# Kernel optimization log

Hardware: AMD Instinct MI355X
Metric: run time of the kernel (lower is better)

## Reference

```python
import jax, jax.numpy as jnp
import numpy as np

B, N, D = 16, 2048, 64

def setup_inputs() -> dict:
    key = jax.random.key(0)
    kq, kk, kv = jax.random.split(key, 3)
    queries = jax.random.normal(kq, (B, N, D), dtype=jnp.float32)
    keys = jax.random.normal(kk, (B, N, D), dtype=jnp.float32)
    values = jax.random.normal(kv, (B, N, D), dtype=jnp.float32)
    scaling_factor = jnp.asarray(np.sqrt(D), dtype=jnp.float32)
    return {"queries": queries, "keys": keys, "values": values, "scaling_factor": scaling_factor}

def reference(queries, keys, values, scaling_factor):
    # scores: [B, N, N] = Q K^T / scale
    scores = jnp.einsum('bqd,bkd->bqk', queries, keys) / scaling_factor
    atn = jax.nn.softmax(scores, axis=2)
    return jnp.einsum('bqk,bkd->bqd', atn, values)
```

## Files before the change

### kernel.cpp

```cpp
#include <hip/hip_runtime.h>
#include <hip/hip_bf16.h>

#define BATCH 16
#define SEQ 2048
#define DIM 64

typedef __attribute__((ext_vector_type(8))) __bf16 bf16x8;
typedef __attribute__((ext_vector_type(8))) unsigned short u16x8;
typedef __attribute__((ext_vector_type(4))) unsigned int u32x4;
typedef __attribute__((ext_vector_type(16))) float f32x16;

#if __has_builtin(__builtin_amdgcn_exp2f)
#define EXP2F(x) __builtin_amdgcn_exp2f(x)
#else
#define EXP2F(x) __expf(0.69314718055994531f * (x))
#endif

__device__ __forceinline__ unsigned short f2bf_hw(float f) {
    __bf16 h = (__bf16)f;
    return __builtin_bit_cast(unsigned short, h);
}

__device__ __forceinline__ unsigned int pk_bf16(float lo, float hi) {
    unsigned int a = f2bf_hw(lo), b = f2bf_hw(hi);
    return a | (b << 16);
}

__device__ __forceinline__ bf16x8 ld_bf8_g(const unsigned short* p) {
    u16x8 u = *(const u16x8*)p;
    return __builtin_bit_cast(bf16x8, u);
}

__global__ __launch_bounds__(256)
void preconvert_kv(const float* __restrict__ K, const float* __restrict__ V,
                   unsigned short* __restrict__ Ks, unsigned short* __restrict__ Vts) {
    __shared__ float vt[128 * 65];
    const int tid = threadIdx.x;
    if (blockIdx.x < 256) {
        const int b = blockIdx.x >> 4;
        const int t = blockIdx.x & 15;
        const float* src = K + ((size_t)(b * SEQ + t * 128)) * DIM;
        unsigned short* dst = Ks + ((size_t)(b * 16 + t)) * 8192;
        #pragma unroll
        for (int p = 0; p < 4; ++p) {
            const int cid = p * 256 + tid;
            const int key = cid >> 3, g = cid & 7;
            const int d0 = (g >> 1) * 16 + (g & 1) * 8;
            float4 x0 = *(const float4*)(src + key * DIM + d0);
            float4 x1 = *(const float4*)(src + key * DIM + d0 + 4);
            u16x8 o;
            o[0] = f2bf_hw(x0.x); o[1] = f2bf_hw(x0.y); o[2] = f2bf_hw(x0.z); o[3] = f2bf_hw(x0.w);
            o[4] = f2bf_hw(x1.x); o[5] = f2bf_hw(x1.y); o[6] = f2bf_hw(x1.z); o[7] = f2bf_hw(x1.w);
            *(u16x8*)(dst + (g * 128 + key) * 8) = o;
        }
    } else {
        const int vb = blockIdx.x - 256;
        const int b = vb >> 4;
        const int t = vb & 15;
        const float* src = V + ((size_t)(b * SEQ + t * 128)) * DIM;
        #pragma unroll
        for (int p = 0; p < 8; ++p) {
            const int f = p * 256 + tid;
            const int row = f >> 4, c4 = (f & 15) << 2;
            float4 x = *(const float4*)(src + row * DIM + c4);
            vt[row * 65 + c4 + 0] = x.x; vt[row * 65 + c4 + 1] = x.y;
            vt[row * 65 + c4 + 2] = x.z; vt[row * 65 + c4 + 3] = x.w;
        }
        __syncthreads();
        unsigned short* dst = Vts + ((size_t)(b * 16 + t)) * 8192;
        #pragma unroll
        for (int p = 0; p < 4; ++p) {
            const int cid = p * 256 + tid;
            const int g = cid >> 6, d = cid & 63;
            const int k0 = (g >> 1) * 16 + (g & 1) * 8;
            u16x8 o;
            #pragma unroll
            for (int j = 0; j < 8; ++j) o[j] = f2bf_hw(vt[(k0 + j) * 65 + d]);
            *(u16x8*)(dst + (g * 64 + d) * 8) = o;
        }
    }
}

__global__ __launch_bounds__(256, 2)
void attn_flash_kernel(const float* __restrict__ Q,
                       const unsigned short* __restrict__ Ks,
                       const unsigned short* __restrict__ Vts,
                       const float* __restrict__ scaling,
                       float* __restrict__ O) {
    __shared__ float comb[3 * 64 * 66];

    const int tid  = threadIdx.x;
    const int w    = tid >> 6;
    const int lane = tid & 63;
    const int m    = lane & 31;
    const int h    = lane >> 5;

    const int x  = blockIdx.x;
    const int b  = ((x & 7) << 1) | ((x >> 3) & 1);
    const int q0 = (x >> 4) * 64;

    const float csc = 1.4426950408889634f / scaling[0];

    bf16x8 aq0[4], aq1[4];
    #pragma unroll
    for (int s = 0; s < 2; ++s) {
        const float* qsrc = Q + ((size_t)(b * SEQ + q0 + s * 32 + m)) * DIM + h * 8;
        #pragma unroll
        for (int c = 0; c < 4; ++c) {
            float4 x0 = *(const float4*)(qsrc + c * 16);
            float4 x1 = *(const float4*)(qsrc + c * 16 + 4);
            u32x4 pk;
            pk[0] = pk_bf16(x0.x * csc, x0.y * csc);
            pk[1] = pk_bf16(x0.z * csc, x0.w * csc);
            pk[2] = pk_bf16(x1.x * csc, x1.y * csc);
            pk[3] = pk_bf16(x1.z * csc, x1.w * csc);
            (s ? aq1 : aq0)[c] = __builtin_bit_cast(bf16x8, pk);
        }
    }

    f32x16 Oacc0[2], Oacc1[2];
    #pragma unroll
    for (int dt = 0; dt < 2; ++dt)
        #pragma unroll
        for (int r = 0; r < 16; ++r) { Oacc0[dt][r] = 0.f; Oacc1[dt][r] = 0.f; }
    float psum0 = 0.f, psum1 = 0.f;

    const unsigned short* Kbase = Ks + ((size_t)(b * 16 + w * 4)) * 8192;
    const unsigned short* Vbase = Vts + ((size_t)(b * 16 + w * 4)) * 8192;

    bf16x8 kc[4];
    #pragma unroll
    for (int c = 0; c < 4; ++c)
        kc[c] = ld_bf8_g(&Kbase[((c * 2 + h) * 128 + m) * 8]);

    #pragma unroll 1
    for (int st = 0; st < 16; ++st) {
        const int it = st >> 2, t = st & 3;
        const unsigned short* Vt = Vbase + (size_t)it * 8192;

        f32x16 S0, S1;
        #pragma unroll
        for (int r = 0; r < 16; ++r) { S0[r] = 0.f; S1[r] = 0.f; }
        #pragma unroll
        for (int c = 0; c < 4; ++c) {
            S0 = __builtin_amdgcn_mfma_f32_32x32x16_bf16(kc[c], aq0[c], S0, 0, 0, 0);
            S1 = __builtin_amdgcn_mfma_f32_32x32x16_bf16(kc[c], aq1[c], S1, 0, 0, 0);
        }

        const int stn = (st < 15) ? st + 1 : 15;
        const unsigned short* Ktn = Kbase + (size_t)(stn >> 2) * 8192;
        const int tn = stn & 3;
        bf16x8 kn[4];
        #pragma unroll
        for (int c = 0; c < 4; ++c)
            kn[c] = ld_bf8_g(&Ktn[((c * 2 + h) * 128 + tn * 32 + m) * 8]);

        bf16x8 bv[2][2];
        #pragma unroll
        for (int c2 = 0; c2 < 2; ++c2)
            #pragma unroll
            for (int dt = 0; dt < 2; ++dt)
                bv[c2][dt] = ld_bf8_g(&Vt[(((2 * t + c2) * 2 + h) * 64 + dt * 32 + m) * 8]);

        unsigned int d0a[8], d0b[8], dsa[8], dsb[8];
        #pragma unroll
        for (int k = 0; k < 4; ++k) {
            float a0 = EXP2F(S0[4 * k + 0]), a1 = EXP2F(S0[4 * k + 1]);
            float a2 = EXP2F(S0[4 * k + 2]), a3 = EXP2F(S0[4 * k + 3]);
            psum0 += (a0 + a1) + (a2 + a3);
            d0a[2 * k + 0] = pk_bf16(a0, a1);
            d0a[2 * k + 1] = pk_bf16(a2, a3);
            float b0 = EXP2F(S1[4 * k + 0]), b1 = EXP2F(S1[4 * k + 1]);
            float b2 = EXP2F(S1[4 * k + 2]), b3 = EXP2F(S1[4 * k + 3]);
            psum1 += (b0 + b1) + (b2 + b3);
            d0b[2 * k + 0] = pk_bf16(b0, b1);
            d0b[2 * k + 1] = pk_bf16(b2, b3);
        }
        #pragma unroll
        for (int i = 0; i < 8; ++i) {
            dsa[i] = (unsigned int)__shfl_xor((int)d0a[i], 32);
            dsb[i] = (unsigned int)__shfl_xor((int)d0b[i], 32);
        }
        #pragma unroll
        for (int c2 = 0; c2 < 2; ++c2) {
            u32x4 bw0, bw1;
            bw0[0] = h ? dsa[4 * c2 + 2] : d0a[4 * c2 + 0];
            bw0[1] = h ? dsa[4 * c2 + 3] : d0a[4 * c2 + 1];
            bw0[2] = h ? d0a[4 * c2 + 2] : dsa[4 * c2 + 0];
            bw0[3] = h ? d0a[4 * c2 + 3] : dsa[4 * c2 + 1];
            bw1[0] = h ? dsb[4 * c2 + 2] : d0b[4 * c2 + 0];
            bw1[1] = h ? dsb[4 * c2 + 3] : d0b[4 * c2 + 1];
            bw1[2] = h ? d0b[4 * c2 + 2] : dsb[4 * c2 + 0];
            bw1[3] = h ? d0b[4 * c2 + 3] : dsb[4 * c2 + 1];
            bf16x8 pb0 = __builtin_bit_cast(bf16x8, bw0);
            bf16x8 pb1 = __builtin_bit_cast(bf16x8, bw1);
            #pragma unroll
            for (int dt = 0; dt < 2; ++dt) {
                Oacc0[dt] = __builtin_amdgcn_mfma_f32_32x32x16_bf16(bv[c2][dt], pb0, Oacc0[dt], 0, 0, 0);
                Oacc1[dt] = __builtin_amdgcn_mfma_f32_32x32x16_bf16(bv[c2][dt], pb1, Oacc1[dt], 0, 0, 0);
            }
        }

        #pragma unroll
        for (int c = 0; c < 4; ++c) kc[c] = kn[c];
    }

    float l0 = psum0 + __shfl_xor(psum0, 32);
    float l1 = psum1 + __shfl_xor(psum1, 32);
    if (w > 0) {
        float* dst = comb + ((w - 1) * 64 + lane) * 66;
        #pragma unroll
        for (int dt = 0; dt < 2; ++dt)
            #pragma unroll
            for (int r = 0; r < 16; ++r) {
                dst[dt * 16 + r]      = Oacc0[dt][r];
                dst[33 + dt * 16 + r] = Oacc1[dt][r];
            }
        dst[32] = l0;
        dst[65] = l1;
    }
    __syncthreads();
    if (w == 0) {
        const float* p0 = comb + (0 * 64 + lane) * 66;
        const float* p1 = comb + (1 * 64 + lane) * 66;
        const float* p2 = comb + (2 * 64 + lane) * 66;
        const float invl0 = 1.0f / (l0 + p0[32] + p1[32] + p2[32]);
        const float invl1 = 1.0f / (l1 + p0[65] + p1[65] + p2[65]);
        float* orow0 = O + ((size_t)(b * SEQ + q0 + m)) * DIM;
        float* orow1 = O + ((size_t)(b * SEQ + q0 + 32 + m)) * DIM;
        #pragma unroll
        for (int dt = 0; dt < 2; ++dt) {
            #pragma unroll
            for (int k = 0; k < 4; ++k) {
                float4 o4;
                #pragma unroll
                for (int j = 0; j < 4; ++j) {
                    const int r = 4 * k + j;
                    ((float*)&o4)[j] = (Oacc0[dt][r] + p0[dt * 16 + r] + p1[dt * 16 + r]
                                        + p2[dt * 16 + r]) * invl0;
                }
                *(float4*)(orow0 + dt * 32 + 8 * k + 4 * h) = o4;
                #pragma unroll
                for (int j = 0; j < 4; ++j) {
                    const int r = 4 * k + j;
                    ((float*)&o4)[j] = (Oacc1[dt][r] + p0[33 + dt * 16 + r] + p1[33 + dt * 16 + r]
                                        + p2[33 + dt * 16 + r]) * invl1;
                }
                *(float4*)(orow1 + dt * 32 + 8 * k + 4 * h) = o4;
            }
        }
    }
}

extern "C" void kernel_launch(void* const* d_in, const int* in_sizes, int n_in,
                              void* d_out, int out_size, void* d_ws, size_t ws_size,
                              hipStream_t stream) {
    const float* Q = (const float*)d_in[0];
    const float* K = (const float*)d_in[1];
    const float* V = (const float*)d_in[2];
    const float* scaling = (const float*)d_in[3];
    float* O = (float*)d_out;

    unsigned short* Ks  = (unsigned short*)d_ws;
    unsigned short* Vts = Ks + (size_t)BATCH * 16 * 8192;

    preconvert_kv<<<dim3(512), dim3(256), 0, stream>>>(K, V, Ks, Vts);
    attn_flash_kernel<<<dim3(BATCH * (SEQ / 64)), dim3(256), 0, stream>>>(Q, Ks, Vts, scaling, O);
}
```

Baseline: 104.4 us.

## Prefetch V one step ahead, use permlane32_swap, and raise MFMA priority

V fragments are now loaded for the next step after the PV MFMAs instead of at the top of the current step, so their global-load latency can overlap the next QK MFMAs and exp work. The lane-half exchange of P fragments replaces 16 shfl_xor calls (ds_bpermute through LDS hardware) plus selects with the gfx950 permlane32_swap builtin when available. s_setprio raises wave priority around the MFMA blocks to improve interleaving across waves. The prefetch costs extra registers per thread, which may reduce occupancy or cause spills.

```diff
diff --git a/kernel.cpp b/kernel.cpp
--- a/kernel.cpp
+++ b/kernel.cpp
@@ -7,6 +7,7 @@
 
 typedef __attribute__((ext_vector_type(8))) __bf16 bf16x8;
 typedef __attribute__((ext_vector_type(8))) unsigned short u16x8;
+typedef __attribute__((ext_vector_type(2))) unsigned int u32x2;
 typedef __attribute__((ext_vector_type(4))) unsigned int u32x4;
 typedef __attribute__((ext_vector_type(16))) float f32x16;
 
@@ -29,6 +30,21 @@
 __device__ __forceinline__ bf16x8 ld_bf8_g(const unsigned short* p) {
     u16x8 u = *(const u16x8*)p;
     return __builtin_bit_cast(bf16x8, u);
+}
+
+__device__ __forceinline__ void half_swap(unsigned int a, unsigned int b,
+                                          unsigned int& lo, unsigned int& hi) {
+#if __has_builtin(__builtin_amdgcn_permlane32_swap)
+    u32x2 r = __builtin_amdgcn_permlane32_swap(a, b, false, false);
+    lo = r[0];
+    hi = r[1];
+#else
+    unsigned int sa = (unsigned int)__shfl_xor((int)a, 32);
+    unsigned int sb = (unsigned int)__shfl_xor((int)b, 32);
+    const bool hh = (threadIdx.x & 32) != 0;
+    lo = hh ? sb : a;
+    hi = hh ? b : sa;
+#endif
 }
 
 __global__ __launch_bounds__(256)
@@ -132,20 +148,25 @@
     #pragma unroll
     for (int c = 0; c < 4; ++c)
         kc[c] = ld_bf8_g(&Kbase[((c * 2 + h) * 128 + m) * 8]);
+    bf16x8 bv[2][2];
+    #pragma unroll
+    for (int c2 = 0; c2 < 2; ++c2)
+        #pragma unroll
+        for (int dt = 0; dt < 2; ++dt)
+            bv[c2][dt] = ld_bf8_g(&Vbase[((c2 * 2 + h) * 64 + dt * 32 + m) * 8]);
 
     #pragma unroll 1
     for (int st = 0; st < 16; ++st) {
-        const int it = st >> 2, t = st & 3;
-        const unsigned short* Vt = Vbase + (size_t)it * 8192;
-
         f32x16 S0, S1;
         #pragma unroll
         for (int r = 0; r < 16; ++r) { S0[r] = 0.f; S1[r] = 0.f; }
+        __builtin_amdgcn_s_setprio(1);
         #pragma unroll
         for (int c = 0; c < 4; ++c) {
             S0 = __builtin_amdgcn_mfma_f32_32x32x16_bf16(kc[c], aq0[c], S0, 0, 0, 0);
             S1 = __builtin_amdgcn_mfma_f32_32x32x16_bf16(kc[c], aq1[c], S1, 0, 0, 0);
         }
+        __builtin_amdgcn_s_setprio(0);
 
         const int stn = (st < 15) ? st + 1 : 15;
         const unsigned short* Ktn = Kbase + (size_t)(stn >> 2) * 8192;
@@ -155,14 +176,7 @@
         for (int c = 0; c < 4; ++c)
             kn[c] = ld_bf8_g(&Ktn[((c * 2 + h) * 128 + tn * 32 + m) * 8]);
 
-        bf16x8 bv[2][2];
-        #pragma unroll
-        for (int c2 = 0; c2 < 2; ++c2)
-            #pragma unroll
-            for (int dt = 0; dt < 2; ++dt)
-                bv[c2][dt] = ld_bf8_g(&Vt[(((2 * t + c2) * 2 + h) * 64 + dt * 32 + m) * 8]);
-
-        unsigned int d0a[8], d0b[8], dsa[8], dsb[8];
+        unsigned int d0a[8], d0b[8];
         #pragma unroll
         for (int k = 0; k < 4; ++k) {
             float a0 = EXP2F(S0[4 * k + 0]), a1 = EXP2F(S0[4 * k + 1]);
@@ -176,30 +190,40 @@
             d0b[2 * k + 0] = pk_bf16(b0, b1);
             d0b[2 * k + 1] = pk_bf16(b2, b3);
         }
-        #pragma unroll
-        for (int i = 0; i < 8; ++i) {
-            dsa[i] = (unsigned int)__shfl_xor((int)d0a[i], 32);
-            dsb[i] = (unsigned int)__shfl_xor((int)d0b[i], 32);
-        }
+
+        bf16x8 pb0[2], pb1[2];
         #pragma unroll
         for (int c2 = 0; c2 < 2; ++c2) {
             u32x4 bw0, bw1;
-            bw0[0] = h ? dsa[4 * c2 + 2] : d0a[4 * c2 + 0];
-            bw0[1] = h ? dsa[4 * c2 + 3] : d0a[4 * c2 + 1];
-            bw0[2] = h ? d0a[4 * c2 + 2] : dsa[4 * c2 + 0];
-            bw0[3] = h ? d0a[4 * c2 + 3] : dsa[4 * c2 + 1];
-            bw1[0] = h ? dsb[4 * c2 + 2] : d0b[4 * c2 + 0];
-            bw1[1] = h ? dsb[4 * c2 + 3] : d0b[4 * c2 + 1];
-            bw1[2] = h ? d0b[4 * c2 + 2] : dsb[4 * c2 + 0];
-            bw1[3] = h ? d0b[4 * c2 + 3] : dsb[4 * c2 + 1];
-            bf16x8 pb0 = __builtin_bit_cast(bf16x8, bw0);
-            bf16x8 pb1 = __builtin_bit_cast(bf16x8, bw1);
+            unsigned int lo, hi;
+            half_swap(d0a[4 * c2 + 0], d0a[4 * c2 + 2], lo, hi);
+            bw0[0] = lo; bw0[2] = hi;
+            half_swap(d0a[4 * c2 + 1], d0a[4 * c2 + 3], lo, hi);
+            bw0[1] = lo; bw0[3] = hi;
+            half_swap(d0b[4 * c2 + 0], d0b[4 * c2 + 2], lo, hi);
+            bw1[0] = lo; bw1[2] = hi;
+            half_swap(d0b[4 * c2 + 1], d0b[4 * c2 + 3], lo, hi);
+            bw1[1] = lo; bw1[3] = hi;
+            pb0[c2] = __builtin_bit_cast(bf16x8, bw0);
+            pb1[c2] = __builtin_bit_cast(bf16x8, bw1);
+        }
+
+        __builtin_amdgcn_s_setprio(1);
+        #pragma unroll
+        for (int c2 = 0; c2 < 2; ++c2)
             #pragma unroll
             for (int dt = 0; dt < 2; ++dt) {
-                Oacc0[dt] = __builtin_amdgcn_mfma_f32_32x32x16_bf16(bv[c2][dt], pb0, Oacc0[dt], 0, 0, 0);
-                Oacc1[dt] = __builtin_amdgcn_mfma_f32_32x32x16_bf16(bv[c2][dt], pb1, Oacc1[dt], 0, 0, 0);
+                Oacc0[dt] = __builtin_amdgcn_mfma_f32_32x32x16_bf16(bv[c2][dt], pb0[c2], Oacc0[dt], 0, 0, 0);
+                Oacc1[dt] = __builtin_amdgcn_mfma_f32_32x32x16_bf16(bv[c2][dt], pb1[c2], Oacc1[dt], 0, 0, 0);
             }
-        }
+        __builtin_amdgcn_s_setprio(0);
+
+        const unsigned short* Vtn = Vbase + (size_t)(stn >> 2) * 8192;
+        #pragma unroll
+        for (int c2 = 0; c2 < 2; ++c2)
+            #pragma unroll
+            for (int dt = 0; dt < 2; ++dt)
+                bv[c2][dt] = ld_bf8_g(&Vtn[(((2 * tn + c2) * 2 + h) * 64 + dt * 32 + m) * 8]);
 
         #pragma unroll
         for (int c = 0; c < 4; ++c) kc[c] = kn[c];
```

Result: faster. 101.1 us (-3.2%).
